# Kernel tuning notes

Hardware: AMD Instinct MI355X
Metric: run time of the kernel (lower is better)

Reference implementation:

```python
import jax, jax.numpy as jnp
import numpy as np

D_MODEL, D_STATE, D_CONV, D_INNER, DT_RANK, K = 96, 16, 3, 192, 6, 4
B, H, W = 1, 64, 64


def setup_inputs() -> dict:
    key = jax.random.key(0)
    ks = jax.random.split(key, 10)
    x = jax.random.normal(ks[0], (B, H, W, D_MODEL), jnp.float32)
    in_proj_w = jax.random.normal(ks[1], (2 * D_INNER, D_MODEL), jnp.float32) * 0.02
    conv_w = jax.random.normal(ks[2], (D_INNER, 1, D_CONV, D_CONV), jnp.float32) * 0.1
    conv_b = jnp.zeros((D_INNER,), jnp.float32)
    x_proj_w = jax.random.normal(ks[3], (K, DT_RANK + 2 * D_STATE, D_INNER), jnp.float32) * 0.02
    dt_std = DT_RANK ** -0.5
    dt_w = jax.random.uniform(ks[4], (K, D_INNER, DT_RANK), jnp.float32, -dt_std, dt_std)
    # dt bias init: inv-softplus of dt ~ logUniform(1e-3, 1e-1)
    u = jax.random.uniform(ks[5], (K, D_INNER), jnp.float32)
    dt = jnp.exp(u * (np.log(0.1) - np.log(0.001)) + np.log(0.001)).clip(1e-4)
    dt_b = dt + jnp.log(-jnp.expm1(-dt))
    A_logs = jnp.log(jnp.broadcast_to(jnp.arange(1, D_STATE + 1, dtype=jnp.float32), (K * D_INNER, D_STATE)))
    Ds = jnp.ones((K * D_INNER,), jnp.float32)
    ln_g = jnp.ones((D_INNER,), jnp.float32)
    ln_b = jnp.zeros((D_INNER,), jnp.float32)
    out_proj_w = jax.random.normal(ks[6], (D_MODEL, D_INNER), jnp.float32) * 0.02
    return dict(x=x, in_proj_w=in_proj_w, conv_w=conv_w, conv_b=conv_b, x_proj_w=x_proj_w,
                dt_w=dt_w, dt_b=dt_b, A_logs=A_logs, Ds=Ds, ln_g=ln_g, ln_b=ln_b,
                out_proj_w=out_proj_w)


def _ss2d(x, in_proj_w, conv_w, conv_b, x_proj_w, dt_w, dt_b, A_logs, Ds, ln_g, ln_b, out_proj_w):
    b, h, w, c = x.shape
    L = h * w
    d = conv_w.shape[0]            # d_inner
    n = A_logs.shape[1]            # d_state
    r = dt_w.shape[2]              # dt_rank
    # in_proj + split
    xz = jnp.einsum('bhwc,ec->bhwe', x, in_proj_w)
    xx, z = xz[..., :d], xz[..., d:]
    # depthwise conv (NCHW) + SiLU
    xc = xx.transpose(0, 3, 1, 2)
    pad = (D_CONV - 1) // 2
    xc = jax.lax.conv_general_dilated(xc, conv_w, (1, 1), [(pad, pad), (pad, pad)],
                                      feature_group_count=d) + conv_b[None, :, None, None]
    xc = jax.nn.silu(xc)
    # 4 scan directions: HW, WH, and their reverses
    x_hw = xc.reshape(b, d, L)
    x_wh = xc.transpose(0, 1, 3, 2).reshape(b, d, L)
    xs = jnp.stack([x_hw, x_wh, x_hw[..., ::-1], x_wh[..., ::-1]], axis=1)  # (b,K,d,L)
    x_dbl = jnp.einsum('bkdl,kcd->bkcl', xs, x_proj_w)
    dts, Bs, Cs = x_dbl[:, :, :r], x_dbl[:, :, r:r + n], x_dbl[:, :, r + n:]
    dts = jnp.einsum('bkrl,kdr->bkdl', dts, dt_w)
    delta = jax.nn.softplus(dts + dt_b[None, :, :, None])        # (b,K,d,L)
    A = -jnp.exp(A_logs).reshape(K, d, n)
    # time-major scanned inputs
    dA = jnp.exp(jnp.einsum('bkdl,kdn->lbkdn', delta, A))        # (L,b,K,d,n)
    dBu = jnp.einsum('bkdl,bknl,bkdl->lbkdn', delta, Bs, xs)
    Ct = Cs.transpose(3, 0, 1, 2)                                # (L,b,K,n)
    def step(hst, inp):
        dA_t, dBu_t, C_t = inp
        hst = dA_t * hst + dBu_t
        return hst, jnp.einsum('bkdn,bkn->bkd', hst, C_t)
    h0 = jnp.zeros((b, K, d, n), jnp.float32)
    _, ys = jax.lax.scan(step, h0, (dA, dBu, Ct))                # ys: (L,b,K,d)
    out_y = ys.transpose(1, 2, 3, 0) + xs * Ds.reshape(K, d)[None, :, :, None]
    # recombine directions
    inv = out_y[:, 2:4][..., ::-1]
    y1 = out_y[:, 0]
    y2 = inv[:, 0]
    wh = out_y[:, 1].reshape(b, d, w, h).transpose(0, 1, 3, 2).reshape(b, d, L)
    invwh = inv[:, 1].reshape(b, d, w, h).transpose(0, 1, 3, 2).reshape(b, d, L)
    y = (y1 + y2 + wh + invwh).transpose(0, 2, 1).reshape(b, h, w, d)
    # LayerNorm (eps=1e-5, torch default)
    mu = y.mean(-1, keepdims=True)
    var = ((y - mu) ** 2).mean(-1, keepdims=True)
    y = (y - mu) * jax.lax.rsqrt(var + 1e-5) * ln_g + ln_b
    y = y * jax.nn.silu(z)
    return jnp.einsum('bhwd,cd->bhwc', y, out_proj_w)


def reference(x, in_proj_w, conv_w, conv_b, x_proj_w, dt_w, dt_b, A_logs, Ds, ln_g, ln_b, out_proj_w):
    return _ss2d(x, in_proj_w, conv_w, conv_b, x_proj_w, dt_w, dt_b, A_logs, Ds, ln_g, ln_b, out_proj_w)
```

## Files before the change

### kernel.cpp

```cpp
#include <hip/hip_runtime.h>
#include <hip/hip_bf16.h>

#define LL 4096
#define DM 96
#define DI 192
#define NS 16
#define RK 6
#define RKP 8
#define KD 4
#define CPROJ 38
#define NC (KD*DI*NS)
#define PT 32
#define WS 196
#define OT 16
#define L2E 1.44269504f

__device__ __forceinline__ float b2f(__hip_bfloat16 v){ return __bfloat162float(v); }

__device__ __forceinline__ void detect_bf16(const unsigned short* __restrict__ xh, int tid, int* sflag){
  if (tid < 64){
    unsigned short u = xh[2*tid];
    int e = (u >> 7) & 0xFF;
    int sane = (e >= 107 && e <= 131) ? 1 : 0;
    unsigned long long m = __ballot(sane);
    if (tid == 0) *sflag = (__popcll(m) >= 32) ? 1 : 0;
  }
}

struct P12 { const void* p[12]; };
__global__ void k_convert_all(P12 ptrs, float* __restrict__ dst) {
  const int off[12] = {0,36864,38592,38784,67968,72576,73344,85632,86400,86592,86784,105216};
  __shared__ int sflag;
  detect_bf16((const unsigned short*)ptrs.p[0], threadIdx.x, &sflag);
  __syncthreads();
  int f = sflag;
  int i = blockIdx.x * 256 + threadIdx.x;
  if (i >= 105216) return;
  int j = 0;
  #pragma unroll
  for (int s = 1; s < 11; s++) if (i >= off[s]) j = s;
  int e = i - off[j];
  const void* src = ptrs.p[j+1];
  if (f) dst[i] = b2f(((const __hip_bfloat16*)src)[e]);
  else   dst[i] = ((const float*)src)[e];
}

__global__ void k_inproj(const void* __restrict__ xraw,
                         const float* __restrict__ w,
                         float* __restrict__ xx, float* __restrict__ z) {
  __shared__ float xr[8*DM];
  __shared__ int sflag;
  int tid = threadIdx.x;
  detect_bf16((const unsigned short*)xraw, tid, &sflag);
  __syncthreads();
  int l0 = blockIdx.x * 8;
  if (sflag){
    const __hip_bfloat16* xb = (const __hip_bfloat16*)xraw + (size_t)l0*DM;
    for (int i = tid; i < 8*DM; i += 384) xr[i] = b2f(xb[i]);
  } else {
    const float* xf = (const float*)xraw + (size_t)l0*DM;
    for (int i = tid; i < 8*DM; i += 384) xr[i] = xf[i];
  }
  __syncthreads();
  int e = tid;
  float acc[8];
  #pragma unroll
  for (int i=0;i<8;i++) acc[i]=0.f;
  const float4* wr4 = (const float4*)(w + (size_t)e*DM);
  #pragma unroll 4
  for (int c4=0;c4<DM/4;c4++){
    float4 wv = wr4[c4];
    int c = c4*4;
    #pragma unroll
    for (int i=0;i<8;i++){
      float a = acc[i];
      a = fmaf(wv.x, xr[i*DM+c  ], a);
      a = fmaf(wv.y, xr[i*DM+c+1], a);
      a = fmaf(wv.z, xr[i*DM+c+2], a);
      a = fmaf(wv.w, xr[i*DM+c+3], a);
      acc[i] = a;
    }
  }
  if (e < DI) {
    #pragma unroll
    for (int i=0;i<8;i++) xx[(l0+i)*DI + e] = acc[i];
  } else {
    int e2 = e - DI;
    #pragma unroll
    for (int i=0;i<8;i++) z[(l0+i)*DI + e2] = acc[i];
  }
}

__global__ void k_conv(const float* __restrict__ xx,
                       const float* __restrict__ cw,
                       const float* __restrict__ cb,
                       float* __restrict__ xc,
                       float* __restrict__ xct) {
  int l = blockIdx.x;
  int d = threadIdx.x;
  int h = l >> 6, w = l & 63;
  float acc = cb[d];
  #pragma unroll
  for (int ki=0; ki<3; ki++){
    int hh = h + ki - 1;
    if ((unsigned)hh >= 64u) continue;
    #pragma unroll
    for (int kj=0;kj<3;kj++){
      int wj = w + kj - 1;
      if ((unsigned)wj >= 64u) continue;
      acc = fmaf(cw[d*9 + ki*3 + kj], xx[(hh*64+wj)*DI + d], acc);
    }
  }
  float v = acc / (1.f + __expf(-acc));
  xc[l*DI + d] = v;
  xct[(((w<<6)|h))*DI + d] = v;
}

__device__ __forceinline__ int dir_map(int k, int t){
  if (k==0) return t;
  if (k==1) return ((t&63)<<6) | (t>>6);
  if (k==2) return 4095 - t;
  int u = 4095 - t; return ((u&63)<<6) | (u>>6);
}

__global__ void __launch_bounds__(256) k_proj(const float* __restrict__ xc,
                       const float* __restrict__ xpw,
                       float* __restrict__ dts,
                       float* __restrict__ Bb, float* __restrict__ Cb) {
  __shared__ float wl[CPROJ*WS];
  __shared__ float xs[PT*WS];
  int b = blockIdx.x;
  int k = b >> 7;
  int t_base = (b & 127) * PT;
  int tid = threadIdx.x;
  for (int idx = tid; idx < CPROJ*DI; idx += 256){
    int cc = idx / DI, j = idx - cc*DI;
    wl[cc*WS + j] = xpw[(k*CPROJ + cc)*DI + j];
  }
  for (int idx = tid; idx < PT*DI; idx += 256){
    int tt = idx / DI, j = idx - tt*DI;
    xs[tt*WS + j] = xc[dir_map(k, t_base + tt)*DI + j];
  }
  __syncthreads();
  int tg = tid & 7;
  int ty = tid >> 3;
  int cc0 = ty;
  int has2 = (ty + 32 < CPROJ);
  int cc1 = has2 ? (ty + 32) : ty;
  float a0x=0.f,a0y=0.f,a0z=0.f,a0w=0.f;
  float a1x=0.f,a1y=0.f,a1z=0.f,a1w=0.f;
  const float4* w0p = (const float4*)&wl[cc0*WS];
  const float4* w1p = (const float4*)&wl[cc1*WS];
  const float4* x0p = (const float4*)&xs[(tg     )*WS];
  const float4* x1p = (const float4*)&xs[(tg +  8)*WS];
  const float4* x2p = (const float4*)&xs[(tg + 16)*WS];
  const float4* x3p = (const float4*)&xs[(tg + 24)*WS];
  #pragma unroll 4
  for (int jc = 0; jc < DI/4; jc++){
    float4 w0 = w0p[jc], w1 = w1p[jc];
    float4 x0 = x0p[jc], x1 = x1p[jc], x2 = x2p[jc], x3 = x3p[jc];
    a0x = fmaf(w0.x,x0.x,fmaf(w0.y,x0.y,fmaf(w0.z,x0.z,fmaf(w0.w,x0.w,a0x))));
    a0y = fmaf(w0.x,x1.x,fmaf(w0.y,x1.y,fmaf(w0.z,x1.z,fmaf(w0.w,x1.w,a0y))));
    a0z = fmaf(w0.x,x2.x,fmaf(w0.y,x2.y,fmaf(w0.z,x2.z,fmaf(w0.w,x2.w,a0z))));
    a0w = fmaf(w0.x,x3.x,fmaf(w0.y,x3.y,fmaf(w0.z,x3.z,fmaf(w0.w,x3.w,a0w))));
    a1x = fmaf(w1.x,x0.x,fmaf(w1.y,x0.y,fmaf(w1.z,x0.z,fmaf(w1.w,x0.w,a1x))));
    a1y = fmaf(w1.x,x1.x,fmaf(w1.y,x1.y,fmaf(w1.z,x1.z,fmaf(w1.w,x1.w,a1y))));
    a1z = fmaf(w1.x,x2.x,fmaf(w1.y,x2.y,fmaf(w1.z,x2.z,fmaf(w1.w,x2.w,a1z))));
    a1w = fmaf(w1.x,x3.x,fmaf(w1.y,x3.y,fmaf(w1.z,x3.z,fmaf(w1.w,x3.w,a1w))));
  }
  float accs0[4] = {a0x,a0y,a0z,a0w};
  float accs1[4] = {a1x,a1y,a1z,a1w};
  #pragma unroll
  for (int i=0;i<4;i++){
    int t = t_base + tg + 8*i;
    size_t kt = (size_t)k*LL + t;
    {
      int cc = cc0; float v = accs0[i];
      if (cc < RK)            dts[kt*RKP + cc] = v;
      else if (cc < RK+NS)    Bb [kt*NS + (cc-RK)] = v;
      else                    Cb [kt*NS + (cc-RK-NS)] = v;
    }
    if (has2){
      int cc = ty + 32; float v = accs1[i];
      if (cc < RK+NS)         Bb [kt*NS + (cc-RK)] = v;
      else                    Cb [kt*NS + (cc-RK-NS)] = v;
    }
  }
}

template<int CHB>
__global__ void __launch_bounds__(256) k_scan1(
                      const float* __restrict__ xc_hw,
                      const float* __restrict__ xc_wh,
                      const float* __restrict__ dts,
                      const float* __restrict__ Bbuf,
                      const float* __restrict__ Cbuf,
                      const float* __restrict__ A_logs,
                      const float* __restrict__ dtw,
                      const float* __restrict__ dtb,
                      float* __restrict__ PH,
                      float* __restrict__ ydir) {
  constexpr int CS = LL >> CHB;
  int b = blockIdx.x;
  int c = b & ((1<<CHB)-1);
  int kg = b >> CHB;
  int k = kg / 3, dg3 = kg - k*3;
  int tid = threadIdx.x;
  int dl = tid >> 2, nq = tid & 3;
  int d = dg3*64 + dl;
  int kd = k*DI + d;
  float4 Al = *(const float4*)&A_logs[kd*NS + nq*4];
  float A0 = -__expf(Al.x)*L2E, A1 = -__expf(Al.y)*L2E;
  float A2 = -__expf(Al.z)*L2E, A3 = -__expf(Al.w)*L2E;
  float bt = dtb[kd];
  float w0 = dtw[kd*RK+0], w1 = dtw[kd*RK+1], w2 = dtw[kd*RK+2];
  float w3 = dtw[kd*RK+3], w4 = dtw[kd*RK+4], w5 = dtw[kd*RK+5];
  const float* dr = dts + ((size_t)k*LL + c*CS)*RKP;
  const float4* bp = (const float4*)(Bbuf + ((size_t)k*LL + c*CS)*NS) + nq;
  const float4* cp = (const float4*)(Cbuf + ((size_t)k*LL + c*CS)*NS) + nq;
  const float* xbase = (k & 1) ? xc_wh : xc_hw;
  int l0 = (k < 2) ? (c*CS) : (4095 - c*CS);
  int lstep = (k < 2) ? DI : -DI;
  const float* xp = xbase + (size_t)l0*DI + d;
  float* yp = ydir + ((size_t)k*LL + c*CS)*DI + d;
  float h0=0.f,h1=0.f,h2=0.f,h3=0.f, cumD=0.f;
  #pragma unroll
  for (int s=0; s<CS; s++){
    float4 lo = *(const float4*)(dr + s*RKP);
    float4 hi = *(const float4*)(dr + s*RKP + 4);
    float v = bt;
    v = fmaf(w0, lo.x, v); v = fmaf(w1, lo.y, v); v = fmaf(w2, lo.z, v);
    v = fmaf(w3, lo.w, v); v = fmaf(w4, hi.x, v); v = fmaf(w5, hi.y, v);
    float sp = (v > 20.f) ? v : __logf(1.f + __expf(v));
    cumD += sp;
    float sx = sp * xp[(ptrdiff_t)s*lstep];
    float4 bv = bp[s*4];
    float4 cv = cp[s*4];
    float a;
    a = exp2f(sp*A0); h0 = fmaf(a, h0, sx*bv.x);
    a = exp2f(sp*A1); h1 = fmaf(a, h1, sx*bv.y);
    a = exp2f(sp*A2); h2 = fmaf(a, h2, sx*bv.z);
    a = exp2f(sp*A3); h3 = fmaf(a, h3, sx*bv.w);
    float y = h0*cv.x + h1*cv.y + h2*cv.z + h3*cv.w;
    y += __shfl_xor(y, 1, 64);
    y += __shfl_xor(y, 2, 64);
    if (nq == 0) yp[s*DI] = y;
  }
  size_t base2 = ((size_t)c*NC + (size_t)kd*NS + nq*4)*2;
  *(float4*)&PH[base2]   = make_float4(exp2f(A0*cumD), h0, exp2f(A1*cumD), h1);
  *(float4*)&PH[base2+4] = make_float4(exp2f(A2*cumD), h2, exp2f(A3*cumD), h3);
}

template<int CHB>
__global__ void __launch_bounds__(256) k_scan2(float2* __restrict__ PH) {
  constexpr int CH = 1 << CHB;
  int idx = blockIdx.x*256 + threadIdx.x;
  float h = 0.f;
  #pragma unroll 8
  for (int c=0;c<CH;c++){
    float2 ph = PH[(size_t)c*NC + idx];
    PH[(size_t)c*NC + idx].y = h;
    h = fmaf(ph.x, h, ph.y);
  }
}

template<int CHB>
__global__ void __launch_bounds__(192) k_corr(
                      const float* __restrict__ Cbuf,
                      const float* __restrict__ dts,
                      const float* __restrict__ A_logs,
                      const float* __restrict__ dtw,
                      const float* __restrict__ dtb,
                      const float2* __restrict__ PH,
                      float* __restrict__ ydir) {
  constexpr int CS = LL >> CHB;
  int b = blockIdx.x;
  int k = b >> CHB;
  int c = b & ((1<<CHB)-1);
  if (c == 0) return;
  int t0 = c*CS;
  int d = threadIdx.x;
  int kd = k*DI + d;
  __shared__ float cs[CS*NS];
  for (int i = d; i < CS*NS; i += 192)
    cs[i] = Cbuf[((size_t)k*LL + t0)*NS + i];
  float bt = dtb[kd];
  float w0 = dtw[kd*RK+0], w1 = dtw[kd*RK+1], w2 = dtw[kd*RK+2];
  float w3 = dtw[kd*RK+3], w4 = dtw[kd*RK+4], w5 = dtw[kd*RK+5];
  float A2[16], he[16];
  {
    const float4* ap = (const float4*)&A_logs[kd*NS];
    const float2* hp = PH + (size_t)c*NC + (size_t)kd*NS;
    #pragma unroll
    for (int i=0;i<4;i++){
      float4 av = ap[i];
      A2[4*i+0] = -__expf(av.x)*L2E; A2[4*i+1] = -__expf(av.y)*L2E;
      A2[4*i+2] = -__expf(av.z)*L2E; A2[4*i+3] = -__expf(av.w)*L2E;
    }
    #pragma unroll
    for (int n=0;n<16;n++) he[n] = hp[n].y;
  }
  __syncthreads();
  const float* dr = dts + ((size_t)k*LL + t0)*RKP;
  float* yp = ydir + ((size_t)k*LL + t0)*DI + d;
  float cumD = 0.f;
  #pragma unroll 4
  for (int s=0; s<CS; s++){
    float4 lo = *(const float4*)(dr + s*RKP);
    float4 hi = *(const float4*)(dr + s*RKP + 4);
    float v = bt;
    v = fmaf(w0, lo.x, v); v = fmaf(w1, lo.y, v); v = fmaf(w2, lo.z, v);
    v = fmaf(w3, lo.w, v); v = fmaf(w4, hi.x, v); v = fmaf(w5, hi.y, v);
    float sp = (v > 20.f) ? v : __logf(1.f + __expf(v));
    cumD += sp;
    float corr = 0.f;
    #pragma unroll
    for (int n=0;n<16;n++)
      corr = fmaf(cs[s*NS+n]*exp2f(A2[n]*cumD), he[n], corr);
    yp[s*DI] += corr;
  }
}

__global__ void __launch_bounds__(192) k_out(
                      const float* __restrict__ ydir,
                      const float* __restrict__ xc,
                      const float* __restrict__ z,
                      const float* __restrict__ Ds,
                      const float* __restrict__ ln_g,
                      const float* __restrict__ ln_b,
                      const float* __restrict__ opw,
                      void* __restrict__ out,
                      const unsigned short* __restrict__ xh) {
  __shared__ float gs[OT*WS];
  __shared__ float ps[2][OT][12];
  __shared__ float mv[2][OT];
  __shared__ int sflag;
  int tid = threadIdx.x;
  int d = tid;
  detect_bf16(xh, tid, &sflag);
  int l0 = blockIdx.x * OT;
  float dsum = Ds[d] + Ds[DI+d] + Ds[2*DI+d] + Ds[3*DI+d];
  #pragma unroll 4
  for (int r=0;r<OT;r++){
    int l = l0 + r;
    int lt = ((l & 63) << 6) | (l >> 6);
    float y = ydir[(size_t)l*DI + d]
            + ydir[((size_t)LL   + lt)*DI + d]
            + ydir[((size_t)2*LL + (4095 - l))*DI + d]
            + ydir[((size_t)3*LL + (4095 - lt))*DI + d];
    gs[r*WS + d] = fmaf(xc[(size_t)l*DI + d], dsum, y);
  }
  __syncthreads();
  {
    int r = tid / 12, lane = tid - r*12;
    float s1 = 0.f, s2 = 0.f;
    for (int j = lane; j < DI; j += 12){
      float v = gs[r*WS + j];
      s1 += v; s2 += v*v;
    }
    ps[0][r][lane] = s1; ps[1][r][lane] = s2;
  }
  __syncthreads();
  if (tid < OT){
    float a = 0.f, bb = 0.f;
    #pragma unroll
    for (int j=0;j<12;j++){ a += ps[0][tid][j]; bb += ps[1][tid][j]; }
    float mu = a * (1.f/192.f);
    float var = bb * (1.f/192.f) - mu*mu;
    mv[0][tid] = mu; mv[1][tid] = rsqrtf(var + 1e-5f);
  }
  __syncthreads();
  float lg = ln_g[d], lb = ln_b[d];
  #pragma unroll 4
  for (int r=0;r<OT;r++){
    float yn = (gs[r*WS + d] - mv[0][r]) * mv[1][r] * lg + lb;
    float zv = z[(size_t)(l0+r)*DI + d];
    gs[r*WS + d] = yn * (zv / (1.f + __expf(-zv)));
  }
  __syncthreads();
  int half = tid / 96;
  int e = tid - half*96;
  int r0 = half*8;
  float acc[8];
  #pragma unroll
  for (int i=0;i<8;i++) acc[i] = 0.f;
  const float4* wrow = (const float4*)(opw + e*DI);
  #pragma unroll 4
  for (int jc = 0; jc < DI/4; jc++){
    float4 w = wrow[jc];
    #pragma unroll
    for (int i=0;i<8;i++){
      float4 gv = *(const float4*)&gs[(r0+i)*WS + jc*4];
      acc[i] = fmaf(w.x,gv.x,fmaf(w.y,gv.y,fmaf(w.z,gv.z,fmaf(w.w,gv.w,acc[i]))));
    }
  }
  int f = sflag;
  #pragma unroll
  for (int i=0;i<8;i++){
    int l = l0 + r0 + i;
    if (f) ((__hip_bfloat16*)out)[l*DM + e] = __float2bfloat16(acc[i]);
    else   ((float*)out)[l*DM + e] = acc[i];
  }
}

extern "C" void kernel_launch(void* const* d_in, const int* in_sizes, int n_in,
                              void* d_out, int out_size, void* d_ws, size_t ws_size,
                              hipStream_t stream) {
  float* ws = (float*)d_ws;
  float* cvt = ws + 16;
  const int off[12] = {0,36864,38592,38784,67968,72576,73344,85632,86400,86592,86784,105216};
  float* c[12];
  c[0] = nullptr;
  for (int i = 1; i < 12; i++) c[i] = cvt + off[i-1];

  float* big    = cvt + 105216;
  float* xx     = big;
  float* z      = xx + (size_t)LL*DI;
  float* xc     = z  + (size_t)LL*DI;
  float* xct    = xc + (size_t)LL*DI;
  float* dts    = xct + (size_t)LL*DI;
  float* Bb     = dts + (size_t)KD*LL*RKP;
  float* Cb     = Bb + (size_t)KD*LL*NS;
  float* PH     = Cb + (size_t)KD*LL*NS;
  size_t need128 = (size_t)(16 + 105216 + 4*786432 + 131072 + 2*262144
                            + 2*128*NC + (size_t)KD*LL*DI) * 4;
  int chBits = (ws_size >= need128) ? 7 : 6;
  int CHn = 1 << chBits;
  float* ydir = PH + 2*(size_t)CHn*NC;

  P12 ptrs;
  for (int i = 0; i < 12; i++) ptrs.p[i] = d_in[i];
  k_convert_all<<<(105216 + 255)/256, 256, 0, stream>>>(ptrs, cvt);

  k_inproj<<<LL/8, 384, 0, stream>>>(d_in[0], c[1], xx, z);
  k_conv<<<LL, DI, 0, stream>>>(xx, c[2], c[3], xc, xct);
  k_proj<<<KD*(LL/PT), 256, 0, stream>>>(xc, c[4], dts, Bb, Cb);
  if (chBits == 7){
    k_scan1<7><<<KD*3*128, 256, 0, stream>>>(xc, xct, dts, Bb, Cb, c[7], c[5], c[6],
                                             PH, ydir);
    k_scan2<7><<<NC/256, 256, 0, stream>>>((float2*)PH);
    k_corr<7><<<KD*128, 192, 0, stream>>>(Cb, dts, c[7], c[5], c[6],
                                          (const float2*)PH, ydir);
  } else {
    k_scan1<6><<<KD*3*64, 256, 0, stream>>>(xc, xct, dts, Bb, Cb, c[7], c[5], c[6],
                                            PH, ydir);
    k_scan2<6><<<NC/256, 256, 0, stream>>>((float2*)PH);
    k_corr<6><<<KD*64, 192, 0, stream>>>(Cb, dts, c[7], c[5], c[6],
                                         (const float2*)PH, ydir);
  }
  k_out<<<LL/OT, 192, 0, stream>>>(ydir, xc, z, c[8], c[9], c[10], c[11], d_out,
                                   (const unsigned short*)d_in[0]);
}
```

Before: 201.3 us.

## Restructure chunked scan into state-only pass and full recompute pass

```diff
diff --git a/kernel.cpp b/kernel.cpp
--- a/kernel.cpp
+++ b/kernel.cpp
@@ -189,66 +189,66 @@
 }
 
 template<int CHB>
-__global__ void __launch_bounds__(256) k_scan1(
+__global__ void __launch_bounds__(192) k_scanA(
                       const float* __restrict__ xc_hw,
                       const float* __restrict__ xc_wh,
                       const float* __restrict__ dts,
                       const float* __restrict__ Bbuf,
-                      const float* __restrict__ Cbuf,
                       const float* __restrict__ A_logs,
                       const float* __restrict__ dtw,
                       const float* __restrict__ dtb,
-                      float* __restrict__ PH,
-                      float* __restrict__ ydir) {
+                      float2* __restrict__ PH) {
   constexpr int CS = LL >> CHB;
+  __shared__ float ds_[CS*RKP];
+  __shared__ float Bs[CS*NS];
   int b = blockIdx.x;
+  int k = b >> CHB;
   int c = b & ((1<<CHB)-1);
-  int kg = b >> CHB;
-  int k = kg / 3, dg3 = kg - k*3;
-  int tid = threadIdx.x;
-  int dl = tid >> 2, nq = tid & 3;
-  int d = dg3*64 + dl;
+  int t0 = c*CS;
+  int d = threadIdx.x;
   int kd = k*DI + d;
-  float4 Al = *(const float4*)&A_logs[kd*NS + nq*4];
-  float A0 = -__expf(Al.x)*L2E, A1 = -__expf(Al.y)*L2E;
-  float A2 = -__expf(Al.z)*L2E, A3 = -__expf(Al.w)*L2E;
+  for (int i = d; i < CS*RKP; i += 192) ds_[i] = dts[((size_t)k*LL + t0)*RKP + i];
+  for (int i = d; i < CS*NS;  i += 192) Bs[i]  = Bbuf[((size_t)k*LL + t0)*NS + i];
   float bt = dtb[kd];
   float w0 = dtw[kd*RK+0], w1 = dtw[kd*RK+1], w2 = dtw[kd*RK+2];
   float w3 = dtw[kd*RK+3], w4 = dtw[kd*RK+4], w5 = dtw[kd*RK+5];
-  const float* dr = dts + ((size_t)k*LL + c*CS)*RKP;
-  const float4* bp = (const float4*)(Bbuf + ((size_t)k*LL + c*CS)*NS) + nq;
-  const float4* cp = (const float4*)(Cbuf + ((size_t)k*LL + c*CS)*NS) + nq;
+  float A2[16], h[16];
+  {
+    const float4* ap = (const float4*)&A_logs[kd*NS];
+    #pragma unroll
+    for (int i=0;i<4;i++){
+      float4 av = ap[i];
+      A2[4*i+0] = -__expf(av.x)*L2E; A2[4*i+1] = -__expf(av.y)*L2E;
+      A2[4*i+2] = -__expf(av.z)*L2E; A2[4*i+3] = -__expf(av.w)*L2E;
+    }
+  }
+  #pragma unroll
+  for (int n=0;n<16;n++) h[n] = 0.f;
+  __syncthreads();
   const float* xbase = (k & 1) ? xc_wh : xc_hw;
-  int l0 = (k < 2) ? (c*CS) : (4095 - c*CS);
+  int l0 = (k < 2) ? t0 : (LL-1 - t0);
   int lstep = (k < 2) ? DI : -DI;
   const float* xp = xbase + (size_t)l0*DI + d;
-  float* yp = ydir + ((size_t)k*LL + c*CS)*DI + d;
-  float h0=0.f,h1=0.f,h2=0.f,h3=0.f, cumD=0.f;
-  #pragma unroll
+  float cumD = 0.f;
+  #pragma unroll 2
   for (int s=0; s<CS; s++){
-    float4 lo = *(const float4*)(dr + s*RKP);
-    float4 hi = *(const float4*)(dr + s*RKP + 4);
+    float4 lo = *(const float4*)(ds_ + s*RKP);
+    float4 hi = *(const float4*)(ds_ + s*RKP + 4);
     float v = bt;
     v = fmaf(w0, lo.x, v); v = fmaf(w1, lo.y, v); v = fmaf(w2, lo.z, v);
     v = fmaf(w3, lo.w, v); v = fmaf(w4, hi.x, v); v = fmaf(w5, hi.y, v);
     float sp = (v > 20.f) ? v : __logf(1.f + __expf(v));
     cumD += sp;
     float sx = sp * xp[(ptrdiff_t)s*lstep];
-    float4 bv = bp[s*4];
-    float4 cv = cp[s*4];
-    float a;
-    a = exp2f(sp*A0); h0 = fmaf(a, h0, sx*bv.x);
-    a = exp2f(sp*A1); h1 = fmaf(a, h1, sx*bv.y);
-    a = exp2f(sp*A2); h2 = fmaf(a, h2, sx*bv.z);
-    a = exp2f(sp*A3); h3 = fmaf(a, h3, sx*bv.w);
-    float y = h0*cv.x + h1*cv.y + h2*cv.z + h3*cv.w;
-    y += __shfl_xor(y, 1, 64);
-    y += __shfl_xor(y, 2, 64);
-    if (nq == 0) yp[s*DI] = y;
-  }
-  size_t base2 = ((size_t)c*NC + (size_t)kd*NS + nq*4)*2;
-  *(float4*)&PH[base2]   = make_float4(exp2f(A0*cumD), h0, exp2f(A1*cumD), h1);
-  *(float4*)&PH[base2+4] = make_float4(exp2f(A2*cumD), h2, exp2f(A3*cumD), h3);
+    #pragma unroll
+    for (int n=0;n<16;n++){
+      float a = exp2f(sp*A2[n]);
+      h[n] = fmaf(a, h[n], sx*Bs[s*NS+n]);
+    }
+  }
+  float2* php = PH + (size_t)c*NC + (size_t)kd*NS;
+  #pragma unroll
+  for (int n=0;n<16;n++) php[n] = make_float2(exp2f(A2[n]*cumD), h[n]);
 }
 
 template<int CHB>
@@ -265,59 +265,77 @@
 }
 
 template<int CHB>
-__global__ void __launch_bounds__(192) k_corr(
+__global__ void __launch_bounds__(192) k_scanB(
+                      const float* __restrict__ xc_hw,
+                      const float* __restrict__ xc_wh,
+                      const float* __restrict__ dts,
+                      const float* __restrict__ Bbuf,
                       const float* __restrict__ Cbuf,
-                      const float* __restrict__ dts,
                       const float* __restrict__ A_logs,
                       const float* __restrict__ dtw,
                       const float* __restrict__ dtb,
                       const float2* __restrict__ PH,
                       float* __restrict__ ydir) {
   constexpr int CS = LL >> CHB;
+  __shared__ float ds_[CS*RKP];
+  __shared__ float Bs[CS*NS];
+  __shared__ float Cs[CS*NS];
   int b = blockIdx.x;
   int k = b >> CHB;
   int c = b & ((1<<CHB)-1);
-  if (c == 0) return;
   int t0 = c*CS;
   int d = threadIdx.x;
   int kd = k*DI + d;
-  __shared__ float cs[CS*NS];
-  for (int i = d; i < CS*NS; i += 192)
-    cs[i] = Cbuf[((size_t)k*LL + t0)*NS + i];
+  for (int i = d; i < CS*RKP; i += 192) ds_[i] = dts[((size_t)k*LL + t0)*RKP + i];
+  for (int i = d; i < CS*NS;  i += 192) Bs[i]  = Bbuf[((size_t)k*LL + t0)*NS + i];
+  for (int i = d; i < CS*NS;  i += 192) Cs[i]  = Cbuf[((size_t)k*LL + t0)*NS + i];
   float bt = dtb[kd];
   float w0 = dtw[kd*RK+0], w1 = dtw[kd*RK+1], w2 = dtw[kd*RK+2];
   float w3 = dtw[kd*RK+3], w4 = dtw[kd*RK+4], w5 = dtw[kd*RK+5];
-  float A2[16], he[16];
+  float A2[16], h[16];
   {
     const float4* ap = (const float4*)&A_logs[kd*NS];
-    const float2* hp = PH + (size_t)c*NC + (size_t)kd*NS;
     #pragma unroll
     for (int i=0;i<4;i++){
       float4 av = ap[i];
       A2[4*i+0] = -__expf(av.x)*L2E; A2[4*i+1] = -__expf(av.y)*L2E;
       A2[4*i+2] = -__expf(av.z)*L2E; A2[4*i+3] = -__expf(av.w)*L2E;
     }
-    #pragma unroll
-    for (int n=0;n<16;n++) he[n] = hp[n].y;
-  }
-  __syncthreads();
-  const float* dr = dts + ((size_t)k*LL + t0)*RKP;
+  }
+  {
+    const float2* hp = PH + (size_t)c*NC + (size_t)kd*NS;
+    #pragma unroll
+    for (int n=0;n<16;n++) h[n] = hp[n].y;
+  }
+  __syncthreads();
+  const float* xbase = (k & 1) ? xc_wh : xc_hw;
+  int l0 = (k < 2) ? t0 : (LL-1 - t0);
+  int lstep = (k < 2) ? DI : -DI;
+  const float* xp = xbase + (size_t)l0*DI + d;
   float* yp = ydir + ((size_t)k*LL + t0)*DI + d;
-  float cumD = 0.f;
-  #pragma unroll 4
+  #pragma unroll 2
   for (int s=0; s<CS; s++){
-    float4 lo = *(const float4*)(dr + s*RKP);
-    float4 hi = *(const float4*)(dr + s*RKP + 4);
+    float4 lo = *(const float4*)(ds_ + s*RKP);
+    float4 hi = *(const float4*)(ds_ + s*RKP + 4);
     float v = bt;
     v = fmaf(w0, lo.x, v); v = fmaf(w1, lo.y, v); v = fmaf(w2, lo.z, v);
     v = fmaf(w3, lo.w, v); v = fmaf(w4, hi.x, v); v = fmaf(w5, hi.y, v);
     float sp = (v > 20.f) ? v : __logf(1.f + __expf(v));
-    cumD += sp;
-    float corr = 0.f;
-    #pragma unroll
-    for (int n=0;n<16;n++)
-      corr = fmaf(cs[s*NS+n]*exp2f(A2[n]*cumD), he[n], corr);
-    yp[s*DI] += corr;
+    float sx = sp * xp[(ptrdiff_t)s*lstep];
+    #pragma unroll
+    for (int n=0;n<16;n++){
+      float a = exp2f(sp*A2[n]);
+      h[n] = fmaf(a, h[n], sx*Bs[s*NS+n]);
+    }
+    float y0=0.f, y1=0.f, y2=0.f, y3=0.f;
+    #pragma unroll
+    for (int n=0;n<4;n++){
+      y0 = fmaf(h[4*n+0], Cs[s*NS+4*n+0], y0);
+      y1 = fmaf(h[4*n+1], Cs[s*NS+4*n+1], y1);
+      y2 = fmaf(h[4*n+2], Cs[s*NS+4*n+2], y2);
+      y3 = fmaf(h[4*n+3], Cs[s*NS+4*n+3], y3);
+    }
+    yp[s*DI] = (y0+y1)+(y2+y3);
   }
 }
 
@@ -436,17 +454,17 @@
   k_conv<<<LL, DI, 0, stream>>>(xx, c[2], c[3], xc, xct);
   k_proj<<<KD*(LL/PT), 256, 0, stream>>>(xc, c[4], dts, Bb, Cb);
   if (chBits == 7){
-    k_scan1<7><<<KD*3*128, 256, 0, stream>>>(xc, xct, dts, Bb, Cb, c[7], c[5], c[6],
-                                             PH, ydir);
+    k_scanA<7><<<KD*128, 192, 0, stream>>>(xc, xct, dts, Bb, c[7], c[5], c[6],
+                                           (float2*)PH);
     k_scan2<7><<<NC/256, 256, 0, stream>>>((float2*)PH);
-    k_corr<7><<<KD*128, 192, 0, stream>>>(Cb, dts, c[7], c[5], c[6],
+    k_scanB<7><<<KD*128, 192, 0, stream>>>(xc, xct, dts, Bb, Cb, c[7], c[5], c[6],
+                                           (const float2*)PH, ydir);
+  } else {
+    k_scanA<6><<<KD*64, 192, 0, stream>>>(xc, xct, dts, Bb, c[7], c[5], c[6],
+                                          (float2*)PH);
+    k_scan2<6><<<NC/256, 256, 0, stream>>>((float2*)PH);
+    k_scanB<6><<<KD*64, 192, 0, stream>>>(xc, xct, dts, Bb, Cb, c[7], c[5], c[6],
                                           (const float2*)PH, ydir);
-  } else {
-    k_scan1<6><<<KD*3*64, 256, 0, stream>>>(xc, xct, dts, Bb, Cb, c[7], c[5], c[6],
-                                            PH, ydir);
-    k_scan2<6><<<NC/256, 256, 0, stream>>>((float2*)PH);
-    k_corr<6><<<KD*64, 192, 0, stream>>>(Cb, dts, c[7], c[5], c[6],
-                                         (const float2*)PH, ydir);
   }
   k_out<<<LL/OT, 192, 0, stream>>>(ydir, xc, z, c[8], c[9], c[10], c[11], d_out,
                                    (const unsigned short*)d_in[0]);
```

After: 206.3 us. 1.02x slower.
